# Kernel tuning notes

Hardware: AMD Instinct MI355X
Metric: run time of the kernel (lower is better)

The kernel has to match this reference:

```python
import jax, jax.numpy as jnp
import numpy as np

B, N, D = 2, 8192, 32
RADIUS2 = 0.03 ** 2
SIM_THRESH = 0.7
MIN_LEAF = 10
EPS = 1e-8


def setup_inputs() -> dict:
    key = jax.random.key(0)
    ks = jax.random.split(key, 5)
    # points scaled to [0, 0.4)^3 so the 0.03 radius finds a few neighbors per point
    points = jax.random.uniform(ks[0], (B, N, 3), dtype=jnp.float32) * 0.4
    embeddings = jax.random.normal(ks[1], (B, N, D), dtype=jnp.float32)
    leaf_mask = jax.random.randint(ks[2], (B, N), 0, 2).astype(jnp.int32)
    # consistency_net: Linear(2D -> D), ReLU, Linear(D -> D); stored as (in, out)
    W1 = jax.random.normal(ks[3], (2 * D, D), dtype=jnp.float32) / np.sqrt(2 * D)
    b1 = jnp.zeros((D,), dtype=jnp.float32)
    W2 = jax.random.normal(ks[4], (D, D), dtype=jnp.float32) / np.sqrt(D)
    b2 = jnp.zeros((D,), dtype=jnp.float32)
    return {"points": points, "embeddings": embeddings, "leaf_mask": leaf_mask,
            "W1": W1, "b1": b1, "W2": W2, "b2": b2}


def reference(points, embeddings, leaf_mask, W1, b1, W2, b2):
    leaf = leaf_mask > 0  # [B,N]
    # squared pairwise distances via ||a||^2 + ||b||^2 - 2 a.b (avoids [B,N,N,3])
    sq = jnp.sum(points * points, axis=-1)  # [B,N]
    d2 = sq[:, :, None] + sq[:, None, :] - 2.0 * jnp.einsum('bnc,bmc->bnm', points, points)
    nb = (d2 < RADIUS2) & leaf[:, None, :]  # neighbor j must be a leaf point
    nb_count = jnp.sum(nb, axis=-1)  # includes self when leaf[i]
    # cosine similarity with per-vector norm clamp (torch F.cosine_similarity eps)
    norms = jnp.maximum(jnp.linalg.norm(embeddings, axis=-1, keepdims=True), EPS)
    en = embeddings / norms
    sim = jnp.einsum('bnd,bmd->bnm', en, en)
    similar = nb & (sim > SIM_THRESH)
    cnt = jnp.sum(similar, axis=-1)  # [B,N]
    w = similar.astype(embeddings.dtype)
    mean_sim = jnp.einsum('bnm,bmd->bnd', w, embeddings) / jnp.maximum(cnt, 1)[..., None]
    combined = jnp.concatenate([embeddings, mean_sim], axis=-1)  # [B,N,2D]
    h = jax.nn.relu(combined @ W1 + b1)
    out = h @ W2 + b2
    batch_ok = (jnp.sum(leaf, axis=-1) >= MIN_LEAF)[:, None]  # skip batches with <10 leaves
    cond = leaf & (nb_count > 1) & (cnt > 0) & batch_ok
    return jnp.where(cond[..., None], out, embeddings)
```

## Files before the change

kernel.cpp:

```cpp
#include <hip/hip_runtime.h>

#define NPTS 8192
#define BN   16384
#define D    32
#define R2   0.0009f
#define SIMT 0.7f
#define RAD  0.03f
#define BLOCK 256
#define PBLOCK 1024
#define PWAVES 16
#define NGRP   (BN / 64)
#define ZBINS 512
#define ZSCALE 1280.0f
#define AFIELDS 34
#define CHUNK 160

#define GLOBAL_AS __attribute__((address_space(1)))
#define LDS_AS    __attribute__((address_space(3)))

__device__ __forceinline__ void g2lds16(const void* g, void* l) {
  __builtin_amdgcn_global_load_lds((const GLOBAL_AS void*)g, (LDS_AS void*)l,
                                   16, 0, 0);
}
__device__ __forceinline__ void g2lds4(const void* g, void* l) {
  __builtin_amdgcn_global_load_lds((const GLOBAL_AS void*)g, (LDS_AS void*)l,
                                   4, 0, 0);
}

__global__ __launch_bounds__(BLOCK) void histscan_kernel(
    const float* __restrict__ pts, const float* __restrict__ emb,
    const int* __restrict__ leaf, float* __restrict__ invn,
    int* __restrict__ histA, int* __restrict__ histL,
    int* __restrict__ leafcnt, unsigned* __restrict__ done,
    int* __restrict__ rsA, int* __restrict__ rsL,
    int* __restrict__ curA, int* __restrict__ curL) {
  const int p = blockIdx.x * BLOCK + threadIdx.x;
  const float z = pts[3 * p + 2];
  int bin = (int)(z * ZSCALE); if (bin > ZBINS - 1) bin = ZBINS - 1;
  const int b = p >> 13;
  const int lf = leaf[p] > 0;
  atomicAdd(&histA[b * ZBINS + bin], 1);
  if (lf) atomicAdd(&histL[b * ZBINS + bin], 1);

  const float4* er = (const float4*)(emb + (size_t)p * D);
  float ss = 0.f;
#pragma unroll
  for (int i = 0; i < D / 4; ++i) {
    float4 v = er[i];
    ss += v.x * v.x + v.y * v.y + v.z * v.z + v.w * v.w;
  }
  invn[p] = 1.0f / fmaxf(sqrtf(ss), 1e-8f);

  const unsigned long long m = __ballot(lf);
  if ((threadIdx.x & 63) == 0) atomicAdd(&leafcnt[b], (int)__popcll(m));

  __shared__ int islast;
  __threadfence();
  if (threadIdx.x == 0) {
    const unsigned t = __hip_atomic_fetch_add(done, 1u, __ATOMIC_ACQ_REL,
                                              __HIP_MEMORY_SCOPE_AGENT);
    islast = (t == gridDim.x - 1);
  }
  __syncthreads();
  if (!islast) return;

  const int wv = threadIdx.x >> 6;
  const int lane = threadIdx.x & 63;
  const int sb = wv & 1;
  const int* __restrict__ h = (wv < 2) ? histA : histL;
  int* __restrict__ rs = (wv < 2) ? rsA : rsL;
  int* __restrict__ cu = (wv < 2) ? curA : curL;
  int carry = 0;
  for (int c = 0; c < ZBINS / 64; ++c) {
    const int idx = c * 64 + lane;
    const int v = __hip_atomic_load(&h[sb * ZBINS + idx], __ATOMIC_RELAXED,
                                    __HIP_MEMORY_SCOPE_AGENT);
    int incl = v;
#pragma unroll
    for (int off = 1; off < 64; off <<= 1) {
      const int t = __shfl_up(incl, off);
      if (lane >= off) incl += t;
    }
    const int excl = carry + incl - v;
    rs[sb * (ZBINS + 1) + idx] = excl;
    cu[sb * ZBINS + idx] = excl;
    carry += __shfl(incl, 63);
  }
  if (lane == 0) rs[sb * (ZBINS + 1) + ZBINS] = carry;
}

__global__ __launch_bounds__(BLOCK) void scatter_kernel(
    const float* __restrict__ pts, const float* __restrict__ emb,
    const int* __restrict__ leaf, const float* __restrict__ invn,
    int* __restrict__ curA, int* __restrict__ curL,
    float4* __restrict__ sortedA, int* __restrict__ permA,
    float4* __restrict__ pts4L, float* __restrict__ invL,
    float* __restrict__ embL) {
  const int p = blockIdx.x * BLOCK + threadIdx.x;
  const float x = pts[3 * p + 0];
  const float y = pts[3 * p + 1];
  const float z = pts[3 * p + 2];
  const float sq = x * x + y * y + z * z;
  const int lf = leaf[p] > 0;
  const float inv = invn[p];
  int bin = (int)(z * ZSCALE); if (bin > ZBINS - 1) bin = ZBINS - 1;
  const int b = p >> 13;

  const int dst = b * NPTS + atomicAdd(&curA[b * ZBINS + bin], 1);
  sortedA[dst] = make_float4(x, y, z, lf ? inv : -inv);
  permA[dst] = p;

  if (lf) {
    const int dl = b * NPTS + atomicAdd(&curL[b * ZBINS + bin], 1);
    pts4L[dl] = make_float4(x, y, z, 0.5f * (sq - R2));
    invL[dl] = inv;
    const float4* __restrict__ s4 = (const float4*)(emb + (size_t)p * D);
    float4* __restrict__ d4 = (float4*)(embL + (size_t)dl * D);
#pragma unroll
    for (int k = 0; k < D / 4; ++k) d4[k] = s4[k];
  }
}

__global__ __launch_bounds__(PBLOCK) void pair_kernel(
    const float4* __restrict__ sortedA, const int* __restrict__ permA,
    const float4* __restrict__ pts4L, const float* __restrict__ invL,
    const float* __restrict__ embL, const float* __restrict__ emb,
    const int* __restrict__ rsL, const int* __restrict__ leafcnt,
    const float* __restrict__ W1, const float* __restrict__ b1,
    const float* __restrict__ W2, const float* __restrict__ b2,
    float* __restrict__ out) {
  const int ig   = blockIdx.x;
  const int b    = ig >> 7;
  const int lane = threadIdx.x & 63;
  const int wv   = threadIdx.x >> 6;
  const int sg   = ig * 64 + lane;

  __shared__ __align__(16) float4 embS[2][CHUNK * 8];
  __shared__ __align__(16) float4 ptsS[2][192];
  __shared__ float invS[2][192];
  __shared__ float red[AFIELDS][64];
  for (int t = threadIdx.x; t < AFIELDS * 64; t += PBLOCK)
    (&red[0][0])[t] = 0.f;

  const float4 A = sortedA[sg];
  const float inv_i = fabsf(A.w);
  const float mhsq = -0.5f * (A.x * A.x + A.y * A.y + A.z * A.z);
  const int p = permA[sg];

  float4 ei[D / 4];
  {
    const float4* __restrict__ e4 = (const float4*)(emb + (size_t)p * D);
#pragma unroll
    for (int k = 0; k < D / 4; ++k) ei[k] = e4[k];
  }

  float zmin = A.z, zmax = A.z;
#pragma unroll
  for (int off = 1; off < 64; off <<= 1) {
    zmin = fminf(zmin, __shfl_xor(zmin, off));
    zmax = fmaxf(zmax, __shfl_xor(zmax, off));
  }
  int klo = (int)((zmin - RAD) * ZSCALE) - 1; if (klo < 0) klo = 0;
  int khi = (int)((zmax + RAD) * ZSCALE) + 1; if (khi > ZBINS - 1) khi = ZBINS - 1;
  klo = __builtin_amdgcn_readfirstlane(klo);
  khi = __builtin_amdgcn_readfirstlane(khi);
  const int jlo = b * NPTS + rsL[b * (ZBINS + 1) + klo];
  const int jhi = b * NPTS + rsL[b * (ZBINS + 1) + khi + 1];
  const int len = jhi - jlo;

  float acc[D];
#pragma unroll
  for (int d = 0; d < D; ++d) acc[d] = 0.f;
  float nbc = 0.f, cnt = 0.f;

  auto stage = [&](int buf, int base, int L) {
    const int nf4 = L * 8;
    for (int t0 = wv * 64; t0 < nf4; t0 += PWAVES * 64)
      g2lds16((const char*)embL + (((size_t)base * 8 + t0 + lane) << 4),
              &embS[buf][t0]);
    for (int t0 = wv * 64; t0 < L; t0 += PWAVES * 64)
      g2lds16((const char*)pts4L + (((size_t)base + t0 + lane) << 4),
              &ptsS[buf][t0]);
    {
      const int t0 = (wv - 4) * 64;
      if (t0 >= 0 && t0 < L)
        g2lds4((const char*)invL + (((size_t)base + t0 + lane) << 2),
               &invS[buf][t0]);
    }
  };

  auto process = [&](int buf, int L) {
    const int s0 = (L * wv) / PWAVES;
    const int s1 = (L * (wv + 1)) / PWAVES;
    if (s0 >= s1) return;
    float4 c = ptsS[buf][s0];
    for (int jl = s0; jl < s1; ++jl) {
      const float4 cn = ptsS[buf][(jl + 1 < s1) ? (jl + 1) : s0];
      const float t = fmaf(A.z, c.z, fmaf(A.y, c.y, fmaf(A.x, c.x, mhsq)));
      if (t > c.w) {
        nbc += 1.0f;
        const float4* __restrict__ ej4 = &embS[buf][jl * 8];
        float s0_ = 0.f, s1_ = 0.f, s2_ = 0.f, s3_ = 0.f;
#pragma unroll
        for (int k = 0; k < D / 4; ++k) {
          const float4 vj = ej4[k];
          s0_ = fmaf(ei[k].x, vj.x, s0_);
          s1_ = fmaf(ei[k].y, vj.y, s1_);
          s2_ = fmaf(ei[k].z, vj.z, s2_);
          s3_ = fmaf(ei[k].w, vj.w, s3_);
        }
        const float sm = ((s0_ + s1_) + (s2_ + s3_)) * inv_i * invS[buf][jl];
        if (sm > SIMT) {
          cnt += 1.0f;
#pragma unroll
          for (int k = 0; k < D / 4; ++k) {
            const float4 vj = ej4[k];
            acc[4 * k + 0] += vj.x;
            acc[4 * k + 1] += vj.y;
            acc[4 * k + 2] += vj.z;
            acc[4 * k + 3] += vj.w;
          }
        }
      }
      c = cn;
    }
  };

  const int nch = (len + CHUNK - 1) / CHUNK;
  if (nch > 0) {
    stage(0, jlo, (len < CHUNK) ? len : CHUNK);
    __syncthreads();
    for (int k = 0; k < nch; ++k) {
      const int cur = k & 1;
      if (k + 1 < nch) {
        const int base = jlo + (k + 1) * CHUNK;
        const int L = (jhi - base < CHUNK) ? (jhi - base) : CHUNK;
        stage(cur ^ 1, base, L);
      }
      const int Lc = (len - k * CHUNK < CHUNK) ? (len - k * CHUNK) : CHUNK;
      process(cur, Lc);
      __syncthreads();
    }
  } else {
    __syncthreads();
  }

  if (nbc != 0.f) atomicAdd(&red[0][lane], nbc);
  if (cnt != 0.f) {
    atomicAdd(&red[1][lane], cnt);
#pragma unroll
    for (int d = 0; d < D; ++d) atomicAdd(&red[2 + d][lane], acc[d]);
  }
  __syncthreads();

  if (threadIdx.x < 64) {
    const float tnbc = red[0][lane];
    const float tcnt = red[1][lane];
    const float rinv = 1.0f / fmaxf(tcnt, 1.0f);

    float e[D];
#pragma unroll
    for (int k = 0; k < D / 4; ++k) {
      e[4 * k + 0] = ei[k].x; e[4 * k + 1] = ei[k].y;
      e[4 * k + 2] = ei[k].z; e[4 * k + 3] = ei[k].w;
    }

    float h[D];
#pragma unroll
    for (int k = 0; k < D; ++k) h[k] = b1[k];
    for (int d = 0; d < D; ++d) {
      const float c = e[d];
      const float* __restrict__ w = W1 + (size_t)d * D;
#pragma unroll
      for (int k = 0; k < D; ++k) h[k] = fmaf(c, w[k], h[k]);
    }
    for (int d = 0; d < D; ++d) {
      const float c = red[2 + d][lane] * rinv;
      const float* __restrict__ w = W1 + (size_t)(D + d) * D;
#pragma unroll
      for (int k = 0; k < D; ++k) h[k] = fmaf(c, w[k], h[k]);
    }
#pragma unroll
    for (int k = 0; k < D; ++k) h[k] = fmaxf(h[k], 0.f);

    float o[D];
#pragma unroll
    for (int m = 0; m < D; ++m) o[m] = b2[m];
    for (int k = 0; k < D; ++k) {
      const float c = h[k];
      const float* __restrict__ w = W2 + (size_t)k * D;
#pragma unroll
      for (int m = 0; m < D; ++m) o[m] = fmaf(c, w[m], o[m]);
    }

    const bool lf = A.w > 0.f;
    const bool cond = lf && (tnbc >= 2.0f) && (tcnt >= 1.0f) && (leafcnt[b] >= 10);

    float4* outr = (float4*)(out + (size_t)p * D);
#pragma unroll
    for (int i = 0; i < D / 4; ++i) {
      float4 v;
      if (cond) { v.x = o[4*i+0]; v.y = o[4*i+1]; v.z = o[4*i+2]; v.w = o[4*i+3]; }
      else      { v = ei[i]; }
      outr[i] = v;
    }
  }
}

extern "C" void kernel_launch(void* const* d_in, const int* in_sizes, int n_in,
                              void* d_out, int out_size, void* d_ws, size_t ws_size,
                              hipStream_t stream) {
  (void)in_sizes; (void)n_in; (void)out_size; (void)ws_size;
  const float* pts  = (const float*)d_in[0];
  const float* emb  = (const float*)d_in[1];
  const int*   leaf = (const int*)d_in[2];
  const float* W1   = (const float*)d_in[3];
  const float* b1   = (const float*)d_in[4];
  const float* W2   = (const float*)d_in[5];
  const float* b2   = (const float*)d_in[6];
  float* out = (float*)d_out;

  char* ws = (char*)d_ws;
  size_t off = 0;
  auto alloc = [&](size_t bytes) { void* r = ws + off; off = (off + bytes + 15) & ~(size_t)15; return r; };

  float4*   sortedA = (float4*)alloc((size_t)BN * 16);
  int*      permA   = (int*)alloc((size_t)BN * 4);
  float4*   pts4L   = (float4*)alloc((size_t)(BN + CHUNK) * 16);
  float*    invL    = (float*)alloc((size_t)(BN + CHUNK) * 4);
  float*    embL    = (float*)alloc((size_t)(BN + CHUNK) * D * 4);
  float*    invn    = (float*)alloc((size_t)BN * 4);
  int*      rsA     = (int*)alloc(2 * (ZBINS + 1) * 4);
  int*      rsL     = (int*)alloc(2 * (ZBINS + 1) * 4);
  int*      curA    = (int*)alloc(2 * ZBINS * 4);
  int*      curL    = (int*)alloc(2 * ZBINS * 4);
  int*      histA   = (int*)alloc(2 * ZBINS * 4);
  int*      histL   = (int*)alloc(2 * ZBINS * 4);
  int*      leafcnt = (int*)alloc(16);
  unsigned* done    = (unsigned*)alloc(16);

  hipMemsetAsync(histA, 0, 2 * (2 * ZBINS * 4) + 32, stream);
  histscan_kernel<<<BN / BLOCK, BLOCK, 0, stream>>>(
      pts, emb, leaf, invn, histA, histL, leafcnt, done, rsA, rsL, curA, curL);
  scatter_kernel<<<BN / BLOCK, BLOCK, 0, stream>>>(
      pts, emb, leaf, invn, curA, curL, sortedA, permA, pts4L, invL, embL);
  pair_kernel<<<NGRP, PBLOCK, 0, stream>>>(
      sortedA, permA, pts4L, invL, embL, emb, rsL, leafcnt,
      W1, b1, W2, b2, out);
}
```

Measured before the change: 134.2 us.

## Compact neighbor hits into per-wave queues and process similarity densely

Each lane no longer runs the cosine-similarity and accumulation branch divergently in the distance loop. Hits are ballot-compacted into a per-wave LDS queue and drained 64 at a time, so all lanes run the dot product together, reading neighbor embeddings from global memory and query embeddings from a swizzled LDS table. Accumulation moves to LDS atomics, and the embedding staging is dropped, which allows a larger chunk of point data per stage. The aim is to remove branch divergence and cut LDS traffic, in exchange for scattered global loads and contended LDS atomics.

```diff
diff --git a/kernel.cpp b/kernel.cpp
--- a/kernel.cpp
+++ b/kernel.cpp
@@ -13,7 +13,7 @@
 #define ZBINS 512
 #define ZSCALE 1280.0f
 #define AFIELDS 34
-#define CHUNK 160
+#define CHUNK 512
 
 #define GLOBAL_AS __attribute__((address_space(1)))
 #define LDS_AS    __attribute__((address_space(3)))
@@ -21,10 +21,6 @@
 __device__ __forceinline__ void g2lds16(const void* g, void* l) {
   __builtin_amdgcn_global_load_lds((const GLOBAL_AS void*)g, (LDS_AS void*)l,
                                    16, 0, 0);
-}
-__device__ __forceinline__ void g2lds4(const void* g, void* l) {
-  __builtin_amdgcn_global_load_lds((const GLOBAL_AS void*)g, (LDS_AS void*)l,
-                                   4, 0, 0);
 }
 
 __global__ __launch_bounds__(BLOCK) void histscan_kernel(
@@ -135,9 +131,10 @@
   const int wv   = threadIdx.x >> 6;
   const int sg   = ig * 64 + lane;
 
-  __shared__ __align__(16) float4 embS[2][CHUNK * 8];
-  __shared__ __align__(16) float4 ptsS[2][192];
-  __shared__ float invS[2][192];
+  __shared__ __align__(16) float4 ptsS[2][CHUNK];
+  __shared__ __align__(16) float4 eiS4[64 * 8];
+  __shared__ float invIS[64];
+  __shared__ int   queueS[PWAVES][128];
   __shared__ float red[AFIELDS][64];
   for (int t = threadIdx.x; t < AFIELDS * 64; t += PBLOCK)
     (&red[0][0])[t] = 0.f;
@@ -147,11 +144,11 @@
   const float mhsq = -0.5f * (A.x * A.x + A.y * A.y + A.z * A.z);
   const int p = permA[sg];
 
-  float4 ei[D / 4];
-  {
+  if (wv == 0) {
     const float4* __restrict__ e4 = (const float4*)(emb + (size_t)p * D);
 #pragma unroll
-    for (int k = 0; k < D / 4; ++k) ei[k] = e4[k];
+    for (int k = 0; k < D / 4; ++k) eiS4[lane * 8 + (k ^ (lane & 7))] = e4[k];
+    invIS[lane] = inv_i;
   }
 
   float zmin = A.z, zmax = A.z;
@@ -168,28 +165,51 @@
   const int jhi = b * NPTS + rsL[b * (ZBINS + 1) + khi + 1];
   const int len = jhi - jlo;
 
-  float acc[D];
-#pragma unroll
-  for (int d = 0; d < D; ++d) acc[d] = 0.f;
-  float nbc = 0.f, cnt = 0.f;
+  float nbc = 0.f;
+  int qtail = 0, qdone = 0;
+
+  const float4* __restrict__ embQ = (const float4*)embL;
+
+  auto drain = [&](int n) {
+    if (lane < n) {
+      const int e  = queueS[wv][(qdone + lane) & 127];
+      const int il = e & 63;
+      const int j  = e >> 6;
+      float4 bv[D / 4];
+#pragma unroll
+      for (int k = 0; k < D / 4; ++k) bv[k] = embQ[(size_t)j * 8 + k];
+      const float invj = invL[j];
+      float s0 = 0.f, s1 = 0.f, s2 = 0.f, s3 = 0.f;
+#pragma unroll
+      for (int k = 0; k < D / 4; ++k) {
+        const float4 av = eiS4[il * 8 + (k ^ (il & 7))];
+        s0 = fmaf(av.x, bv[k].x, s0);
+        s1 = fmaf(av.y, bv[k].y, s1);
+        s2 = fmaf(av.z, bv[k].z, s2);
+        s3 = fmaf(av.w, bv[k].w, s3);
+      }
+      const float sim = ((s0 + s1) + (s2 + s3)) * invIS[il] * invj;
+      if (sim > SIMT) {
+        atomicAdd(&red[1][il], 1.0f);
+#pragma unroll
+        for (int k = 0; k < D / 4; ++k) {
+          atomicAdd(&red[2 + 4 * k + 0][il], bv[k].x);
+          atomicAdd(&red[2 + 4 * k + 1][il], bv[k].y);
+          atomicAdd(&red[2 + 4 * k + 2][il], bv[k].z);
+          atomicAdd(&red[2 + 4 * k + 3][il], bv[k].w);
+        }
+      }
+    }
+    qdone += n;
+  };
 
   auto stage = [&](int buf, int base, int L) {
-    const int nf4 = L * 8;
-    for (int t0 = wv * 64; t0 < nf4; t0 += PWAVES * 64)
-      g2lds16((const char*)embL + (((size_t)base * 8 + t0 + lane) << 4),
-              &embS[buf][t0]);
     for (int t0 = wv * 64; t0 < L; t0 += PWAVES * 64)
-      g2lds16((const char*)pts4L + (((size_t)base + t0 + lane) << 4),
+      g2lds16((const char*)pts4L + (((size_t)(base + t0 + lane)) << 4),
               &ptsS[buf][t0]);
-    {
-      const int t0 = (wv - 4) * 64;
-      if (t0 >= 0 && t0 < L)
-        g2lds4((const char*)invL + (((size_t)base + t0 + lane) << 2),
-               &invS[buf][t0]);
-    }
   };
 
-  auto process = [&](int buf, int L) {
+  auto process = [&](int buf, int jbase, int L) {
     const int s0 = (L * wv) / PWAVES;
     const int s1 = (L * (wv + 1)) / PWAVES;
     if (s0 >= s1) return;
@@ -197,60 +217,39 @@
     for (int jl = s0; jl < s1; ++jl) {
       const float4 cn = ptsS[buf][(jl + 1 < s1) ? (jl + 1) : s0];
       const float t = fmaf(A.z, c.z, fmaf(A.y, c.y, fmaf(A.x, c.x, mhsq)));
-      if (t > c.w) {
-        nbc += 1.0f;
-        const float4* __restrict__ ej4 = &embS[buf][jl * 8];
-        float s0_ = 0.f, s1_ = 0.f, s2_ = 0.f, s3_ = 0.f;
-#pragma unroll
-        for (int k = 0; k < D / 4; ++k) {
-          const float4 vj = ej4[k];
-          s0_ = fmaf(ei[k].x, vj.x, s0_);
-          s1_ = fmaf(ei[k].y, vj.y, s1_);
-          s2_ = fmaf(ei[k].z, vj.z, s2_);
-          s3_ = fmaf(ei[k].w, vj.w, s3_);
+      const bool hit = t > c.w;
+      const unsigned long long m = __ballot(hit);
+      if (m) {
+        if (hit) {
+          nbc += 1.0f;
+          const int below = __popcll(m & ((1ull << lane) - 1ull));
+          queueS[wv][(qtail + below) & 127] = ((jbase + jl) << 6) | lane;
         }
-        const float sm = ((s0_ + s1_) + (s2_ + s3_)) * inv_i * invS[buf][jl];
-        if (sm > SIMT) {
-          cnt += 1.0f;
-#pragma unroll
-          for (int k = 0; k < D / 4; ++k) {
-            const float4 vj = ej4[k];
-            acc[4 * k + 0] += vj.x;
-            acc[4 * k + 1] += vj.y;
-            acc[4 * k + 2] += vj.z;
-            acc[4 * k + 3] += vj.w;
-          }
-        }
+        qtail += (int)__popcll(m);
+        if (qtail - qdone >= 64) drain(64);
       }
       c = cn;
     }
   };
 
   const int nch = (len + CHUNK - 1) / CHUNK;
-  if (nch > 0) {
-    stage(0, jlo, (len < CHUNK) ? len : CHUNK);
+  if (nch > 0) stage(0, jlo, (len < CHUNK) ? len : CHUNK);
+  __syncthreads();
+  for (int k = 0; k < nch; ++k) {
+    const int cur = k & 1;
+    if (k + 1 < nch) {
+      const int base = jlo + (k + 1) * CHUNK;
+      const int L = (jhi - base < CHUNK) ? (jhi - base) : CHUNK;
+      stage(cur ^ 1, base, L);
+    }
+    const int base = jlo + k * CHUNK;
+    const int Lc = (jhi - base < CHUNK) ? (jhi - base) : CHUNK;
+    process(cur, base, Lc);
     __syncthreads();
-    for (int k = 0; k < nch; ++k) {
-      const int cur = k & 1;
-      if (k + 1 < nch) {
-        const int base = jlo + (k + 1) * CHUNK;
-        const int L = (jhi - base < CHUNK) ? (jhi - base) : CHUNK;
-        stage(cur ^ 1, base, L);
-      }
-      const int Lc = (len - k * CHUNK < CHUNK) ? (len - k * CHUNK) : CHUNK;
-      process(cur, Lc);
-      __syncthreads();
-    }
-  } else {
-    __syncthreads();
-  }
+  }
+  drain(qtail - qdone);
 
   if (nbc != 0.f) atomicAdd(&red[0][lane], nbc);
-  if (cnt != 0.f) {
-    atomicAdd(&red[1][lane], cnt);
-#pragma unroll
-    for (int d = 0; d < D; ++d) atomicAdd(&red[2 + d][lane], acc[d]);
-  }
   __syncthreads();
 
   if (threadIdx.x < 64) {
@@ -261,8 +260,9 @@
     float e[D];
 #pragma unroll
     for (int k = 0; k < D / 4; ++k) {
-      e[4 * k + 0] = ei[k].x; e[4 * k + 1] = ei[k].y;
-      e[4 * k + 2] = ei[k].z; e[4 * k + 3] = ei[k].w;
+      const float4 v = eiS4[lane * 8 + (k ^ (lane & 7))];
+      e[4 * k + 0] = v.x; e[4 * k + 1] = v.y;
+      e[4 * k + 2] = v.z; e[4 * k + 3] = v.w;
     }
 
     float h[D];
@@ -301,7 +301,7 @@
     for (int i = 0; i < D / 4; ++i) {
       float4 v;
       if (cond) { v.x = o[4*i+0]; v.y = o[4*i+1]; v.z = o[4*i+2]; v.w = o[4*i+3]; }
-      else      { v = ei[i]; }
+      else      { v.x = e[4*i+0]; v.y = e[4*i+1]; v.z = e[4*i+2]; v.w = e[4*i+3]; }
       outr[i] = v;
     }
   }
```

Result: faster. 115.1 us (-14.3%).
